# Kernel optimization log

Hardware: AMD Instinct MI355X
Metric: run time of the kernel (lower is better)

Reference implementation:

```python
import jax, jax.numpy as jnp
import numpy as np

NPOINT = 512
NSAMPLE = 32
RADIUS = 0.2


def furthest_point_sampling(pts, npoint):
    # pts: (B, N, 3) -> (B, npoint) int32 indices
    B, N, _ = pts.shape

    def step(carry, _):
        dist, far = carry  # (B,N), (B,)
        centroid = jnp.take_along_axis(pts, far[:, None, None], axis=1)  # (B,1,3)
        d2 = jnp.sum((pts - centroid) ** 2, axis=-1)  # (B,N)
        dist = jnp.minimum(dist, d2)
        nfar = jnp.argmax(dist, axis=-1).astype(jnp.int32)
        return (dist, nfar), far

    init = (jnp.full((B, N), 1e10, pts.dtype), jnp.zeros((B,), jnp.int32))
    _, idxs = jax.lax.scan(step, init, None, length=npoint)
    return idxs.T  # (B, npoint)


def ball_query(new_xyz, xyz, nsample, radius):
    # new_xyz: (B,S,3), xyz: (B,N,3) -> (B,S,nsample) int32
    N = xyz.shape[1]
    d2 = jnp.sum((new_xyz[:, :, None, :] - xyz[:, None, :, :]) ** 2, axis=-1)  # (B,S,N)
    ar = jnp.arange(N, dtype=jnp.int32)
    key = jnp.where(d2 < radius * radius, ar, N)  # valid idx, else sentinel N
    idx = jnp.sort(key, axis=-1)[..., :nsample]  # first nsample in-radius indices
    first = idx[..., :1]
    idx = jnp.where(idx == N, first, idx)  # pad with first valid (CUDA ball_query behavior)
    return jnp.minimum(idx, N - 1)


def group_points(feat, idx):
    # feat: (B,C,N), idx: (B,S,K) -> (B,C,S,K)
    return jax.vmap(lambda f, i: f[:, i])(feat, idx)


def pointnet_sa(xyz, features, W1, b1, W2, b2, W3, b3):
    xyz_t = jnp.transpose(xyz, (0, 2, 1))  # (B,N,3)
    fps_idx = furthest_point_sampling(xyz_t, NPOINT)  # (B,S)
    new_xyz = group_points(xyz, fps_idx[:, :, None])[..., 0]  # (B,3,S)
    idx = ball_query(jnp.transpose(new_xyz, (0, 2, 1)), xyz_t, NSAMPLE, RADIUS)  # (B,S,K)
    grouped_xyz = group_points(xyz, idx) - new_xyz[:, :, :, None]  # (B,3,S,K), centered
    grouped_feat = group_points(features, idx)  # (B,C,S,K)
    h = jnp.concatenate([grouped_xyz, grouped_feat], axis=1)  # (B,C+3,S,K)
    for W, b in ((W1, b1), (W2, b2), (W3, b3)):
        h = jax.nn.relu(jnp.einsum('oc,bcsk->bosk', W, h) + b[None, :, None, None])
    new_features = jnp.max(h, axis=3)  # (B,out,S)
    return new_xyz, new_features


def setup_inputs() -> dict:
    key = jax.random.key(0)
    ks = jax.random.split(key, 8)
    B, N, C = 16, 2048, 64
    return {
        'xyz': jax.random.uniform(ks[0], (B, 3, N), dtype=jnp.float32),
        'features': jax.random.normal(ks[1], (B, C, N), dtype=jnp.float32),
        'W1': jax.random.normal(ks[2], (64, 67), dtype=jnp.float32) * 0.1,
        'b1': jnp.zeros((64,), jnp.float32),
        'W2': jax.random.normal(ks[3], (128, 64), dtype=jnp.float32) * 0.1,
        'b2': jnp.zeros((128,), jnp.float32),
        'W3': jax.random.normal(ks[4], (256, 128), dtype=jnp.float32) * 0.1,
        'b3': jnp.zeros((256,), jnp.float32),
    }


def reference(xyz, features, W1, b1, W2, b2, W3, b3):
    return pointnet_sa(xyz, features, W1, b1, W2, b2, W3, b3)
```

## Files before the change

kernel.cpp:

```cpp
#include <hip/hip_runtime.h>

#define NB 16
#define NN 2048
#define NP 512
#define NS 32
#define NC 64

typedef _Float16 f16x8 __attribute__((ext_vector_type(8)));
typedef _Float16 f16x4 __attribute__((ext_vector_type(4)));
typedef float f32x4 __attribute__((ext_vector_type(4)));
typedef float f32x2 __attribute__((ext_vector_type(2)));

__device__ __forceinline__ float sqdist(float dx, float dy, float dz) {
  return __fadd_rn(__fadd_rn(__fmul_rn(dx, dx), __fmul_rn(dy, dy)), __fmul_rn(dz, dz));
}

__device__ __forceinline__ f32x2 pk_add(f32x2 a, f32x2 b) {
  f32x2 d;
  asm("v_pk_add_f32 %0, %1, %2" : "=v"(d) : "v"(a), "v"(b));
  return d;
}
__device__ __forceinline__ f32x2 pk_mul(f32x2 a, f32x2 b) {
  f32x2 d;
  asm("v_pk_mul_f32 %0, %1, %2" : "=v"(d) : "v"(a), "v"(b));
  return d;
}

template <int CTRL>
__device__ __forceinline__ float dppmaxf(float m) {
  int t = __builtin_amdgcn_update_dpp(0, __float_as_int(m), CTRL, 0xf, 0xf, true);
  return fmaxf(m, __int_as_float(t));
}

__global__ __launch_bounds__(256, 1) void front_kernel(
    const float* __restrict__ xyz, const float* __restrict__ feat,
    const float* __restrict__ W1, const float* __restrict__ W2, const float* __restrict__ W3,
    float* __restrict__ newxyz, _Float16* __restrict__ featF, float* __restrict__ xyzT,
    _Float16* __restrict__ W1f, _Float16* __restrict__ W2f, _Float16* __restrict__ W3f) {
  __shared__ __align__(16) char sm[32896];
  const int bid = blockIdx.x;
  const int t = threadIdx.x;

  if (bid >= 16) {
    if (bid == 528) {
      for (int i = t; i < 256 * 128; i += 256) {
        if (i < 64 * 96) {
          int o = i / 96, k = i - o * 96;
          float v = (k < 64) ? W1[o * 67 + 3 + k] : ((k < 67) ? W1[o * 67 + (k - 64)] : 0.f);
          W1f[i] = (_Float16)v;
        }
        if (i < 128 * 64) W2f[i] = (_Float16)W2[i];
        W3f[i] = (_Float16)W3[i];
      }
      return;
    }
    float(*tile)[65] = (float(*)[65])sm;
    const int pb = bid - 16;
    const int b = pb >> 5;
    const int n0 = (pb & 31) * 64;
    const int g = t >> 6, l = t & 63;
    if (g == 0) {
      int n = n0 + l;
      float4 q;
      q.x = xyz[(size_t)b * 3 * NN + n];
      q.y = xyz[(size_t)b * 3 * NN + NN + n];
      q.z = xyz[(size_t)b * 3 * NN + 2 * NN + n];
      q.w = 0.f;
      ((float4*)xyzT)[(size_t)b * NN + n] = q;
    }
#pragma unroll
    for (int r = 0; r < 16; ++r) {
      int c = g * 16 + r;
      tile[c][l] = feat[((size_t)b * NC + c) * NN + n0 + l];
    }
    __syncthreads();
#pragma unroll
    for (int r = 0; r < 16; ++r) {
      int nl = g * 16 + r;
      featF[((size_t)(b * NN + n0 + nl)) * NC + l] = (_Float16)tile[l][nl];
    }
    return;
  }

  const int b = bid;
  const int w = t >> 6;
  const float* X = xyz + (size_t)b * 3 * NN;
  float4* XL = (float4*)sm;
  uint2* ck = (uint2*)(sm + 32768);

  f32x2 px[4], py[4], pz[4], dist[4];
#pragma unroll
  for (int jj = 0; jj < 4; ++jj) {
    int n0 = t + 256 * jj, n1 = n0 + 1024;
    px[jj] = f32x2{X[n0], X[n1]};
    py[jj] = f32x2{X[NN + n0], X[NN + n1]};
    pz[jj] = f32x2{X[2 * NN + n0], X[2 * NN + n1]};
    dist[jj] = f32x2{1e10f, 1e10f};
    XL[n0] = make_float4(px[jj].x, py[jj].x, pz[jj].x, 0.f);
    XL[n1] = make_float4(px[jj].y, py[jj].y, pz[jj].y, 0.f);
  }
  float cx = X[0], cy = X[NN], cz = X[2 * NN];
  __syncthreads();
  int buf = 0;
  for (int i = 0; i < NP; ++i) {
    if (t == 0) {
      newxyz[b * 3 * NP + i] = cx;
      newxyz[b * 3 * NP + NP + i] = cy;
      newxyz[b * 3 * NP + 2 * NP + i] = cz;
    }
    const f32x2 ncx = f32x2{-cx, -cx}, ncy = f32x2{-cy, -cy}, ncz = f32x2{-cz, -cz};
    float hm[4];
#pragma unroll
    for (int jj = 0; jj < 4; ++jj) {
      f32x2 dx = pk_add(px[jj], ncx);
      f32x2 dy = pk_add(py[jj], ncy);
      f32x2 dz = pk_add(pz[jj], ncz);
      f32x2 s = pk_add(pk_add(pk_mul(dx, dx), pk_mul(dy, dy)), pk_mul(dz, dz));
      f32x2 d = dist[jj];
      d.x = fminf(d.x, s.x);
      d.y = fminf(d.y, s.y);
      dist[jj] = d;
      hm[jj] = fmaxf(d.x, d.y);
    }
    float m = fmaxf(fmaxf(hm[0], hm[1]), fmaxf(hm[2], hm[3]));
    m = dppmaxf<0x111>(m);
    m = dppmaxf<0x112>(m);
    m = dppmaxf<0x114>(m);
    m = dppmaxf<0x118>(m);
    m = dppmaxf<0x142>(m);
    m = dppmaxf<0x143>(m);
    const float vmax = __int_as_float(__builtin_amdgcn_readlane(__float_as_int(m), 63));
    unsigned long long mm[8];
#pragma unroll
    for (int jj = 0; jj < 4; ++jj) {
      mm[jj] = __ballot(dist[jj].x == vmax);
      mm[4 + jj] = __ballot(dist[jj].y == vmax);
    }
    unsigned nw = 0;
#pragma unroll
    for (int q = 7; q >= 0; --q)
      if (mm[q]) nw = 256u * (unsigned)q + (unsigned)(w << 6) + (unsigned)__builtin_ctzll(mm[q]);
    if ((t & 63) == 0) ck[buf * 4 + w] = make_uint2(__float_as_uint(vmax), nw);
    __syncthreads();
    uint4 c01 = *(const uint4*)&ck[buf * 4 + 0];
    uint4 c23 = *(const uint4*)&ck[buf * 4 + 2];
    unsigned v = c01.x, n = c01.y;
    if (c01.z > v || (c01.z == v && c01.w < n)) { v = c01.z; n = c01.w; }
    if (c23.x > v || (c23.x == v && c23.y < n)) { v = c23.x; n = c23.y; }
    if (c23.z > v || (c23.z == v && c23.w < n)) { v = c23.z; n = c23.w; }
    float4 c = XL[n];
    cx = c.x;
    cy = c.y;
    cz = c.z;
    buf ^= 1;
  }
}

#define HSTR 104
#define A1STR 72
#define A2STR 136
#define A1OFF 17408

__global__ __launch_bounds__(256) void mlp_kernel(
    const float* __restrict__ xyz, const float* __restrict__ xyzT,
    const _Float16* __restrict__ featF, const float* __restrict__ newxyz,
    const _Float16* __restrict__ W1f, const float* __restrict__ b1,
    const _Float16* __restrict__ W2f, const float* __restrict__ b2,
    const _Float16* __restrict__ W3f, const float* __restrict__ b3, float* __restrict__ out) {
  __shared__ _Float16 smem[17408 + 9216];
  __shared__ int idx_l[4][32];
  __shared__ float cxyz[4][4];
  _Float16* hT = smem;
  _Float16* a1T = smem + A1OFF;
  const int b = blockIdx.x;
  const int s0 = blockIdx.y * 4;
  const int t = threadIdx.x;
  const int lane = t & 63, w = t >> 6;

  {
    const float* X = xyz + (size_t)b * 3 * NN;
    const int sW = s0 + w;
    const float cxw = newxyz[b * 3 * NP + sW];
    const float cyw = newxyz[b * 3 * NP + NP + sW];
    const float czw = newxyz[b * 3 * NP + 2 * NP + sW];
    if (lane == 0) {
      cxyz[w][0] = cxw;
      cxyz[w][1] = cyw;
      cxyz[w][2] = czw;
    }
    const float r2 = (float)(0.2 * 0.2);
    int total = 0, first = 0;
    bool havefirst = false;
    for (int c0 = 0; c0 < NN; c0 += 64) {
      int n = c0 + lane;
      float d2 = sqdist(X[n] - cxw, X[NN + n] - cyw, X[2 * NN + n] - czw);
      bool hit = d2 < r2;
      unsigned long long mask = __ballot(hit);
      if (!havefirst && mask) {
        first = c0 + __builtin_ctzll(mask);
        havefirst = true;
      }
      if (hit) {
        int pos = total + (int)__popcll(mask & ((1ull << lane) - 1ull));
        if (pos < NS) idx_l[w][pos] = n;
      }
      total += (int)__popcll(mask);
      if (total >= NS) break;
    }
    if (total < NS && lane >= total && lane < NS) idx_l[w][lane] = first;
  }
  __syncthreads();

  {
    const int col = t & 127, hf = t >> 7;
    const int n = idx_l[col >> 5][col & 31];
    const _Float16* F = featF + (size_t)(b * NN + n) * NC;
#pragma unroll
    for (int j = 0; j < 4; ++j) {
      int p = hf * 4 + j;
      *(f16x8*)(&hT[col * HSTR + p * 8]) = *(const f16x8*)(F + p * 8);
    }
    if (hf == 0) {
      float4 pnt = ((const float4*)xyzT)[(size_t)b * NN + n];
      f16x8 v = {};
      v[0] = (_Float16)(pnt.x - cxyz[col >> 5][0]);
      v[1] = (_Float16)(pnt.y - cxyz[col >> 5][1]);
      v[2] = (_Float16)(pnt.z - cxyz[col >> 5][2]);
      *(f16x8*)(&hT[col * HSTR + 64]) = v;
    } else {
      f16x8 z = {};
      *(f16x8*)(&hT[col * HSTR + 72]) = z;
      *(f16x8*)(&hT[col * HSTR + 80]) = z;
      *(f16x8*)(&hT[col * HSTR + 88]) = z;
    }
  }
  __syncthreads();

  const int cl = lane & 15;
  const int kg = lane >> 4;

  {
    f32x4 acc[8];
    {
      f32x4 bb = *(const f32x4*)(b1 + w * 16 + kg * 4);
#pragma unroll
      for (int ct = 0; ct < 8; ++ct) acc[ct] = bb;
    }
#pragma unroll
    for (int ks = 0; ks < 3; ++ks) {
      f16x8 A = *(const f16x8*)(W1f + (w * 16 + cl) * 96 + ks * 32 + kg * 8);
#pragma unroll
      for (int ct = 0; ct < 8; ++ct) {
        f16x8 B = *(const f16x8*)(&hT[(ct * 16 + cl) * HSTR + ks * 32 + kg * 8]);
        acc[ct] = __builtin_amdgcn_mfma_f32_16x16x32_f16(A, B, acc[ct], 0, 0, 0);
      }
    }
#pragma unroll
    for (int ct = 0; ct < 8; ++ct) {
      f16x4 v;
#pragma unroll
      for (int i2 = 0; i2 < 4; ++i2) v[i2] = (_Float16)fmaxf(acc[ct][i2], 0.f);
      *(f16x4*)(&a1T[(ct * 16 + cl) * A1STR + w * 16 + kg * 4]) = v;
    }
  }
  __syncthreads();

  {
    f32x4 acc[2][8];
#pragma unroll
    for (int r = 0; r < 2; ++r) {
      f32x4 bb = *(const f32x4*)(b2 + w * 32 + r * 16 + kg * 4);
#pragma unroll
      for (int ct = 0; ct < 8; ++ct) acc[r][ct] = bb;
    }
#pragma unroll
    for (int ks = 0; ks < 2; ++ks) {
      f16x8 A0 = *(const f16x8*)(W2f + (w * 32 + cl) * 64 + ks * 32 + kg * 8);
      f16x8 A1 = *(const f16x8*)(W2f + (w * 32 + 16 + cl) * 64 + ks * 32 + kg * 8);
#pragma unroll
      for (int ct = 0; ct < 8; ++ct) {
        f16x8 B = *(const f16x8*)(&a1T[(ct * 16 + cl) * A1STR + ks * 32 + kg * 8]);
        acc[0][ct] = __builtin_amdgcn_mfma_f32_16x16x32_f16(A0, B, acc[0][ct], 0, 0, 0);
        acc[1][ct] = __builtin_amdgcn_mfma_f32_16x16x32_f16(A1, B, acc[1][ct], 0, 0, 0);
      }
    }
#pragma unroll
    for (int r = 0; r < 2; ++r)
#pragma unroll
      for (int ct = 0; ct < 8; ++ct) {
        f16x4 v;
#pragma unroll
        for (int i2 = 0; i2 < 4; ++i2) v[i2] = (_Float16)fmaxf(acc[r][ct][i2], 0.f);
        *(f16x4*)(&hT[(ct * 16 + cl) * A2STR + w * 32 + r * 16 + kg * 4]) = v;
      }
  }
  __syncthreads();

  float* out2 = out + NB * 3 * NP;
#pragma unroll
  for (int rh = 0; rh < 2; ++rh) {
    f32x4 acc[2][8];
#pragma unroll
    for (int r = 0; r < 2; ++r) {
      f32x4 bb = *(const f32x4*)(b3 + w * 64 + rh * 32 + r * 16 + kg * 4);
#pragma unroll
      for (int ct = 0; ct < 8; ++ct) acc[r][ct] = bb;
    }
#pragma unroll
    for (int ks = 0; ks < 4; ++ks) {
      f16x8 A0 = *(const f16x8*)(W3f + (w * 64 + rh * 32 + cl) * 128 + ks * 32 + kg * 8);
      f16x8 A1 = *(const f16x8*)(W3f + (w * 64 + rh * 32 + 16 + cl) * 128 + ks * 32 + kg * 8);
#pragma unroll
      for (int ct = 0; ct < 8; ++ct) {
        f16x8 B = *(const f16x8*)(&hT[(ct * 16 + cl) * A2STR + ks * 32 + kg * 8]);
        acc[0][ct] = __builtin_amdgcn_mfma_f32_16x16x32_f16(A0, B, acc[0][ct], 0, 0, 0);
        acc[1][ct] = __builtin_amdgcn_mfma_f32_16x16x32_f16(A1, B, acc[1][ct], 0, 0, 0);
      }
    }
#pragma unroll
    for (int r = 0; r < 2; ++r)
#pragma unroll
      for (int sl = 0; sl < 4; ++sl) {
        float vv[4];
#pragma unroll
        for (int i2 = 0; i2 < 4; ++i2) {
          float m0 = fmaxf(acc[r][sl * 2][i2], 0.f);
          float m1 = fmaxf(acc[r][sl * 2 + 1][i2], 0.f);
          float mv = fmaxf(m0, m1);
          mv = fmaxf(mv, __shfl_xor(mv, 1, 64));
          mv = fmaxf(mv, __shfl_xor(mv, 2, 64));
          mv = fmaxf(mv, __shfl_xor(mv, 4, 64));
          mv = fmaxf(mv, __shfl_xor(mv, 8, 64));
          vv[i2] = mv;
        }
        if (cl == 0) {
          int ob = w * 64 + rh * 32 + r * 16 + kg * 4;
#pragma unroll
          for (int i2 = 0; i2 < 4; ++i2)
            out2[((size_t)(b * 256 + ob + i2)) * NP + s0 + sl] = vv[i2];
        }
      }
  }
}

extern "C" void kernel_launch(void* const* d_in, const int* in_sizes, int n_in, void* d_out,
                              int out_size, void* d_ws, size_t ws_size, hipStream_t stream) {
  const float* xyz = (const float*)d_in[0];
  const float* feat = (const float*)d_in[1];
  const float* W1 = (const float*)d_in[2];
  const float* b1 = (const float*)d_in[3];
  const float* W2 = (const float*)d_in[4];
  const float* b2 = (const float*)d_in[5];
  const float* W3 = (const float*)d_in[6];
  const float* b3 = (const float*)d_in[7];
  float* out = (float*)d_out;
  char* ws = (char*)d_ws;
  float* xyzT = (float*)ws;
  _Float16* featF = (_Float16*)(ws + 524288);
  _Float16* W1f = (_Float16*)(ws + 4718592);
  _Float16* W2f = (_Float16*)(ws + 4730880);
  _Float16* W3f = (_Float16*)(ws + 4747264);

  hipLaunchKernelGGL(front_kernel, dim3(529), dim3(256), 0, stream, xyz, feat, W1, W2, W3, out,
                     featF, xyzT, W1f, W2f, W3f);
  hipLaunchKernelGGL(mlp_kernel, dim3(NB, 128), dim3(256), 0, stream, xyz, xyzT, featF, out, W1f,
                     b1, W2f, b2, W3f, b3, out);
}
```

Baseline: 388.6 us.

## Fuse FPS and MLP into persistent kernel with counter-based streaming of centroids

Merges the sampling/preprocessing kernel and the grouping+MLP kernel into one persistent kernel of 512 blocks. The 16 FPS blocks publish centroids every 64 iterations through release counters. The other blocks first do the feature transpose and weight conversion, then pull MLP work items from an atomic queue and spin-wait until the needed centroids exist. This lets ball query and the MLP run alongside the serial FPS loop instead of after it. The cost is spin-wait overhead, atomics, and reliance on all blocks being co-resident; it also adds a small init kernel to reset the counters.

```diff
diff --git a/kernel.cpp b/kernel.cpp
--- a/kernel.cpp
+++ b/kernel.cpp
@@ -5,6 +5,7 @@
 #define NP 512
 #define NS 32
 #define NC 64
+#define NWORK 496
 
 typedef _Float16 f16x8 __attribute__((ext_vector_type(8)));
 typedef _Float16 f16x4 __attribute__((ext_vector_type(4)));
@@ -32,17 +33,153 @@
   return fmaxf(m, __int_as_float(t));
 }
 
-__global__ __launch_bounds__(256, 1) void front_kernel(
+__device__ __forceinline__ unsigned ld_relax(const unsigned* p) {
+  return __hip_atomic_load(p, __ATOMIC_RELAXED, __HIP_MEMORY_SCOPE_AGENT);
+}
+__device__ __forceinline__ void waitge(const unsigned* p, unsigned need) {
+  if (ld_relax(p) < need) {
+    unsigned spins = 0;
+    while (ld_relax(p) < need) {
+      __builtin_amdgcn_s_sleep(8);
+      if (++spins > (1u << 22)) break;
+    }
+  }
+  (void)__hip_atomic_load(p, __ATOMIC_ACQUIRE, __HIP_MEMORY_SCOPE_AGENT);
+}
+
+__global__ void init_kernel(unsigned* ctr) {
+  if (threadIdx.x < 18) ctr[threadIdx.x * 16] = 0;
+}
+
+#define HSTR 104
+#define A1STR 72
+#define A2STR 136
+#define A1OFF 17408
+
+__global__ __launch_bounds__(256, 2) void fused_kernel(
     const float* __restrict__ xyz, const float* __restrict__ feat,
-    const float* __restrict__ W1, const float* __restrict__ W2, const float* __restrict__ W3,
-    float* __restrict__ newxyz, _Float16* __restrict__ featF, float* __restrict__ xyzT,
-    _Float16* __restrict__ W1f, _Float16* __restrict__ W2f, _Float16* __restrict__ W3f) {
-  __shared__ __align__(16) char sm[32896];
+    const float* __restrict__ W1, const float* __restrict__ b1, const float* __restrict__ W2,
+    const float* __restrict__ b2, const float* __restrict__ W3, const float* __restrict__ b3,
+    float* __restrict__ out, _Float16* __restrict__ featF, float* __restrict__ xyzT,
+    _Float16* __restrict__ W1f, _Float16* __restrict__ W2f, _Float16* __restrict__ W3f,
+    unsigned* __restrict__ ctr) {
+  __shared__ __align__(16) char sm[53824];
+  __shared__ unsigned mitem;
   const int bid = blockIdx.x;
   const int t = threadIdx.x;
-
-  if (bid >= 16) {
-    if (bid == 528) {
+  float* newxyz = out;
+
+  if (bid < NB) {
+    const int b = bid;
+    const int w = t >> 6;
+    const float* X = xyz + (size_t)b * 3 * NN;
+    float4* XL = (float4*)sm;
+    uint2* ck = (uint2*)(sm + 32768);
+
+    f32x2 px[4], py[4], pz[4], dist[4];
+#pragma unroll
+    for (int jj = 0; jj < 4; ++jj) {
+      int n0 = t + 256 * jj, n1 = n0 + 1024;
+      px[jj] = f32x2{X[n0], X[n1]};
+      py[jj] = f32x2{X[NN + n0], X[NN + n1]};
+      pz[jj] = f32x2{X[2 * NN + n0], X[2 * NN + n1]};
+      dist[jj] = f32x2{1e10f, 1e10f};
+      XL[n0] = make_float4(px[jj].x, py[jj].x, pz[jj].x, 0.f);
+      XL[n1] = make_float4(px[jj].y, py[jj].y, pz[jj].y, 0.f);
+    }
+    float cx = X[0], cy = X[NN], cz = X[2 * NN];
+    __syncthreads();
+    int buf = 0;
+    for (int i = 0; i < NP; ++i) {
+      if (t == 0) {
+        __hip_atomic_store(&newxyz[b * 3 * NP + i], cx, __ATOMIC_RELAXED,
+                           __HIP_MEMORY_SCOPE_AGENT);
+        __hip_atomic_store(&newxyz[b * 3 * NP + NP + i], cy, __ATOMIC_RELAXED,
+                           __HIP_MEMORY_SCOPE_AGENT);
+        __hip_atomic_store(&newxyz[b * 3 * NP + 2 * NP + i], cz, __ATOMIC_RELAXED,
+                           __HIP_MEMORY_SCOPE_AGENT);
+        if ((i & 63) == 63)
+          __hip_atomic_store(&ctr[b * 16], (unsigned)(i + 1), __ATOMIC_RELEASE,
+                             __HIP_MEMORY_SCOPE_AGENT);
+      }
+      const f32x2 ncx = f32x2{-cx, -cx}, ncy = f32x2{-cy, -cy}, ncz = f32x2{-cz, -cz};
+      float hm[4];
+#pragma unroll
+      for (int jj = 0; jj < 4; ++jj) {
+        f32x2 dx = pk_add(px[jj], ncx);
+        f32x2 dy = pk_add(py[jj], ncy);
+        f32x2 dz = pk_add(pz[jj], ncz);
+        f32x2 s = pk_add(pk_add(pk_mul(dx, dx), pk_mul(dy, dy)), pk_mul(dz, dz));
+        f32x2 d = dist[jj];
+        d.x = fminf(d.x, s.x);
+        d.y = fminf(d.y, s.y);
+        dist[jj] = d;
+        hm[jj] = fmaxf(d.x, d.y);
+      }
+      float m = fmaxf(fmaxf(hm[0], hm[1]), fmaxf(hm[2], hm[3]));
+      m = dppmaxf<0x111>(m);
+      m = dppmaxf<0x112>(m);
+      m = dppmaxf<0x114>(m);
+      m = dppmaxf<0x118>(m);
+      m = dppmaxf<0x142>(m);
+      m = dppmaxf<0x143>(m);
+      const float vmax = __int_as_float(__builtin_amdgcn_readlane(__float_as_int(m), 63));
+      unsigned long long mm[8];
+#pragma unroll
+      for (int jj = 0; jj < 4; ++jj) {
+        mm[jj] = __ballot(dist[jj].x == vmax);
+        mm[4 + jj] = __ballot(dist[jj].y == vmax);
+      }
+      unsigned nw = 0;
+#pragma unroll
+      for (int q = 7; q >= 0; --q)
+        if (mm[q]) nw = 256u * (unsigned)q + (unsigned)(w << 6) + (unsigned)__builtin_ctzll(mm[q]);
+      if ((t & 63) == 0) ck[buf * 4 + w] = make_uint2(__float_as_uint(vmax), nw);
+      __syncthreads();
+      uint4 c01 = *(const uint4*)&ck[buf * 4 + 0];
+      uint4 c23 = *(const uint4*)&ck[buf * 4 + 2];
+      unsigned v = c01.x, n = c01.y;
+      if (c01.z > v || (c01.z == v && c01.w < n)) { v = c01.z; n = c01.w; }
+      if (c23.x > v || (c23.x == v && c23.y < n)) { v = c23.x; n = c23.y; }
+      if (c23.z > v || (c23.z == v && c23.w < n)) { v = c23.z; n = c23.w; }
+      float4 c = XL[n];
+      cx = c.x;
+      cy = c.y;
+      cz = c.z;
+      buf ^= 1;
+    }
+  } else {
+    const int wid = bid - NB;
+    for (int rep = 0; rep < 2; ++rep) {
+      int p = wid + rep * NWORK;
+      if (p >= 512) break;
+      float(*tile)[65] = (float(*)[65])sm;
+      const int b = p >> 5;
+      const int n0 = (p & 31) * 64;
+      const int g = t >> 6, l = t & 63;
+      if (g == 0) {
+        int n = n0 + l;
+        float4 q;
+        q.x = xyz[(size_t)b * 3 * NN + n];
+        q.y = xyz[(size_t)b * 3 * NN + NN + n];
+        q.z = xyz[(size_t)b * 3 * NN + 2 * NN + n];
+        q.w = 0.f;
+        ((float4*)xyzT)[(size_t)b * NN + n] = q;
+      }
+      __syncthreads();
+#pragma unroll
+      for (int r = 0; r < 16; ++r) {
+        int c = g * 16 + r;
+        tile[c][l] = feat[((size_t)b * NC + c) * NN + n0 + l];
+      }
+      __syncthreads();
+#pragma unroll
+      for (int r = 0; r < 16; ++r) {
+        int nl = g * 16 + r;
+        featF[((size_t)(b * NN + n0 + nl)) * NC + l] = (_Float16)tile[l][nl];
+      }
+    }
+    if (wid == 31) {
       for (int i = t; i < 256 * 128; i += 256) {
         if (i < 64 * 96) {
           int o = i / 96, k = i - o * 96;
@@ -52,294 +189,199 @@
         if (i < 128 * 64) W2f[i] = (_Float16)W2[i];
         W3f[i] = (_Float16)W3[i];
       }
-      return;
-    }
-    float(*tile)[65] = (float(*)[65])sm;
-    const int pb = bid - 16;
-    const int b = pb >> 5;
-    const int n0 = (pb & 31) * 64;
-    const int g = t >> 6, l = t & 63;
-    if (g == 0) {
-      int n = n0 + l;
-      float4 q;
-      q.x = xyz[(size_t)b * 3 * NN + n];
-      q.y = xyz[(size_t)b * 3 * NN + NN + n];
-      q.z = xyz[(size_t)b * 3 * NN + 2 * NN + n];
-      q.w = 0.f;
-      ((float4*)xyzT)[(size_t)b * NN + n] = q;
-    }
-#pragma unroll
-    for (int r = 0; r < 16; ++r) {
-      int c = g * 16 + r;
-      tile[c][l] = feat[((size_t)b * NC + c) * NN + n0 + l];
-    }
-    __syncthreads();
-#pragma unroll
-    for (int r = 0; r < 16; ++r) {
-      int nl = g * 16 + r;
-      featF[((size_t)(b * NN + n0 + nl)) * NC + l] = (_Float16)tile[l][nl];
-    }
-    return;
+    }
+    __syncthreads();
+    if (t == 0)
+      (void)__hip_atomic_fetch_add(&ctr[16 * 16], 1u, __ATOMIC_RELEASE,
+                                   __HIP_MEMORY_SCOPE_AGENT);
   }
 
-  const int b = bid;
-  const int w = t >> 6;
-  const float* X = xyz + (size_t)b * 3 * NN;
-  float4* XL = (float4*)sm;
-  uint2* ck = (uint2*)(sm + 32768);
-
-  f32x2 px[4], py[4], pz[4], dist[4];
-#pragma unroll
-  for (int jj = 0; jj < 4; ++jj) {
-    int n0 = t + 256 * jj, n1 = n0 + 1024;
-    px[jj] = f32x2{X[n0], X[n1]};
-    py[jj] = f32x2{X[NN + n0], X[NN + n1]};
-    pz[jj] = f32x2{X[2 * NN + n0], X[2 * NN + n1]};
-    dist[jj] = f32x2{1e10f, 1e10f};
-    XL[n0] = make_float4(px[jj].x, py[jj].x, pz[jj].x, 0.f);
-    XL[n1] = make_float4(px[jj].y, py[jj].y, pz[jj].y, 0.f);
-  }
-  float cx = X[0], cy = X[NN], cz = X[2 * NN];
+  if (t == 0) waitge(&ctr[16 * 16], NWORK);
   __syncthreads();
-  int buf = 0;
-  for (int i = 0; i < NP; ++i) {
-    if (t == 0) {
-      newxyz[b * 3 * NP + i] = cx;
-      newxyz[b * 3 * NP + NP + i] = cy;
-      newxyz[b * 3 * NP + 2 * NP + i] = cz;
-    }
-    const f32x2 ncx = f32x2{-cx, -cx}, ncy = f32x2{-cy, -cy}, ncz = f32x2{-cz, -cz};
-    float hm[4];
-#pragma unroll
-    for (int jj = 0; jj < 4; ++jj) {
-      f32x2 dx = pk_add(px[jj], ncx);
-      f32x2 dy = pk_add(py[jj], ncy);
-      f32x2 dz = pk_add(pz[jj], ncz);
-      f32x2 s = pk_add(pk_add(pk_mul(dx, dx), pk_mul(dy, dy)), pk_mul(dz, dz));
-      f32x2 d = dist[jj];
-      d.x = fminf(d.x, s.x);
-      d.y = fminf(d.y, s.y);
-      dist[jj] = d;
-      hm[jj] = fmaxf(d.x, d.y);
-    }
-    float m = fmaxf(fmaxf(hm[0], hm[1]), fmaxf(hm[2], hm[3]));
-    m = dppmaxf<0x111>(m);
-    m = dppmaxf<0x112>(m);
-    m = dppmaxf<0x114>(m);
-    m = dppmaxf<0x118>(m);
-    m = dppmaxf<0x142>(m);
-    m = dppmaxf<0x143>(m);
-    const float vmax = __int_as_float(__builtin_amdgcn_readlane(__float_as_int(m), 63));
-    unsigned long long mm[8];
-#pragma unroll
-    for (int jj = 0; jj < 4; ++jj) {
-      mm[jj] = __ballot(dist[jj].x == vmax);
-      mm[4 + jj] = __ballot(dist[jj].y == vmax);
-    }
-    unsigned nw = 0;
-#pragma unroll
-    for (int q = 7; q >= 0; --q)
-      if (mm[q]) nw = 256u * (unsigned)q + (unsigned)(w << 6) + (unsigned)__builtin_ctzll(mm[q]);
-    if ((t & 63) == 0) ck[buf * 4 + w] = make_uint2(__float_as_uint(vmax), nw);
-    __syncthreads();
-    uint4 c01 = *(const uint4*)&ck[buf * 4 + 0];
-    uint4 c23 = *(const uint4*)&ck[buf * 4 + 2];
-    unsigned v = c01.x, n = c01.y;
-    if (c01.z > v || (c01.z == v && c01.w < n)) { v = c01.z; n = c01.w; }
-    if (c23.x > v || (c23.x == v && c23.y < n)) { v = c23.x; n = c23.y; }
-    if (c23.z > v || (c23.z == v && c23.w < n)) { v = c23.z; n = c23.w; }
-    float4 c = XL[n];
-    cx = c.x;
-    cy = c.y;
-    cz = c.z;
-    buf ^= 1;
-  }
-}
-
-#define HSTR 104
-#define A1STR 72
-#define A2STR 136
-#define A1OFF 17408
-
-__global__ __launch_bounds__(256) void mlp_kernel(
-    const float* __restrict__ xyz, const float* __restrict__ xyzT,
-    const _Float16* __restrict__ featF, const float* __restrict__ newxyz,
-    const _Float16* __restrict__ W1f, const float* __restrict__ b1,
-    const _Float16* __restrict__ W2f, const float* __restrict__ b2,
-    const _Float16* __restrict__ W3f, const float* __restrict__ b3, float* __restrict__ out) {
-  __shared__ _Float16 smem[17408 + 9216];
-  __shared__ int idx_l[4][32];
-  __shared__ float cxyz[4][4];
-  _Float16* hT = smem;
-  _Float16* a1T = smem + A1OFF;
-  const int b = blockIdx.x;
-  const int s0 = blockIdx.y * 4;
-  const int t = threadIdx.x;
+
+  _Float16* hT = (_Float16*)sm;
+  _Float16* a1T = (_Float16*)(sm) + A1OFF;
+  int(*idx_l)[32] = (int(*)[32])(sm + 53248);
+  float(*cxyz)[4] = (float(*)[4])(sm + 53760);
   const int lane = t & 63, w = t >> 6;
-
-  {
-    const float* X = xyz + (size_t)b * 3 * NN;
-    const int sW = s0 + w;
-    const float cxw = newxyz[b * 3 * NP + sW];
-    const float cyw = newxyz[b * 3 * NP + NP + sW];
-    const float czw = newxyz[b * 3 * NP + 2 * NP + sW];
-    if (lane == 0) {
-      cxyz[w][0] = cxw;
-      cxyz[w][1] = cyw;
-      cxyz[w][2] = czw;
-    }
-    const float r2 = (float)(0.2 * 0.2);
-    int total = 0, first = 0;
-    bool havefirst = false;
-    for (int c0 = 0; c0 < NN; c0 += 64) {
-      int n = c0 + lane;
-      float d2 = sqdist(X[n] - cxw, X[NN + n] - cyw, X[2 * NN + n] - czw);
-      bool hit = d2 < r2;
-      unsigned long long mask = __ballot(hit);
-      if (!havefirst && mask) {
-        first = c0 + __builtin_ctzll(mask);
-        havefirst = true;
-      }
-      if (hit) {
-        int pos = total + (int)__popcll(mask & ((1ull << lane) - 1ull));
-        if (pos < NS) idx_l[w][pos] = n;
-      }
-      total += (int)__popcll(mask);
-      if (total >= NS) break;
-    }
-    if (total < NS && lane >= total && lane < NS) idx_l[w][lane] = first;
-  }
-  __syncthreads();
-
-  {
-    const int col = t & 127, hf = t >> 7;
-    const int n = idx_l[col >> 5][col & 31];
-    const _Float16* F = featF + (size_t)(b * NN + n) * NC;
-#pragma unroll
-    for (int j = 0; j < 4; ++j) {
-      int p = hf * 4 + j;
-      *(f16x8*)(&hT[col * HSTR + p * 8]) = *(const f16x8*)(F + p * 8);
-    }
-    if (hf == 0) {
-      float4 pnt = ((const float4*)xyzT)[(size_t)b * NN + n];
-      f16x8 v = {};
-      v[0] = (_Float16)(pnt.x - cxyz[col >> 5][0]);
-      v[1] = (_Float16)(pnt.y - cxyz[col >> 5][1]);
-      v[2] = (_Float16)(pnt.z - cxyz[col >> 5][2]);
-      *(f16x8*)(&hT[col * HSTR + 64]) = v;
-    } else {
-      f16x8 z = {};
-      *(f16x8*)(&hT[col * HSTR + 72]) = z;
-      *(f16x8*)(&hT[col * HSTR + 80]) = z;
-      *(f16x8*)(&hT[col * HSTR + 88]) = z;
-    }
-  }
-  __syncthreads();
-
   const int cl = lane & 15;
   const int kg = lane >> 4;
-
-  {
-    f32x4 acc[8];
+  float* out2 = out + NB * 3 * NP;
+
+  for (;;) {
+    if (t == 0)
+      mitem = __hip_atomic_fetch_add(&ctr[17 * 16], 1u, __ATOMIC_RELAXED,
+                                     __HIP_MEMORY_SCOPE_AGENT);
+    __syncthreads();
+    const unsigned m = mitem;
+    if (m >= (unsigned)(NB * 128)) break;
+    const int b = (int)(m & 15u);
+    const int sg = (int)(m >> 4);
+    const int s0 = sg * 4;
+    if (t == 0) waitge(&ctr[b * 16], (unsigned)(s0 + 4));
+    __syncthreads();
+
     {
-      f32x4 bb = *(const f32x4*)(b1 + w * 16 + kg * 4);
-#pragma unroll
-      for (int ct = 0; ct < 8; ++ct) acc[ct] = bb;
-    }
-#pragma unroll
-    for (int ks = 0; ks < 3; ++ks) {
-      f16x8 A = *(const f16x8*)(W1f + (w * 16 + cl) * 96 + ks * 32 + kg * 8);
-#pragma unroll
-      for (int ct = 0; ct < 8; ++ct) {
-        f16x8 B = *(const f16x8*)(&hT[(ct * 16 + cl) * HSTR + ks * 32 + kg * 8]);
-        acc[ct] = __builtin_amdgcn_mfma_f32_16x16x32_f16(A, B, acc[ct], 0, 0, 0);
-      }
-    }
-#pragma unroll
-    for (int ct = 0; ct < 8; ++ct) {
-      f16x4 v;
-#pragma unroll
-      for (int i2 = 0; i2 < 4; ++i2) v[i2] = (_Float16)fmaxf(acc[ct][i2], 0.f);
-      *(f16x4*)(&a1T[(ct * 16 + cl) * A1STR + w * 16 + kg * 4]) = v;
-    }
-  }
-  __syncthreads();
-
-  {
-    f32x4 acc[2][8];
-#pragma unroll
-    for (int r = 0; r < 2; ++r) {
-      f32x4 bb = *(const f32x4*)(b2 + w * 32 + r * 16 + kg * 4);
-#pragma unroll
-      for (int ct = 0; ct < 8; ++ct) acc[r][ct] = bb;
-    }
-#pragma unroll
-    for (int ks = 0; ks < 2; ++ks) {
-      f16x8 A0 = *(const f16x8*)(W2f + (w * 32 + cl) * 64 + ks * 32 + kg * 8);
-      f16x8 A1 = *(const f16x8*)(W2f + (w * 32 + 16 + cl) * 64 + ks * 32 + kg * 8);
-#pragma unroll
-      for (int ct = 0; ct < 8; ++ct) {
-        f16x8 B = *(const f16x8*)(&a1T[(ct * 16 + cl) * A1STR + ks * 32 + kg * 8]);
-        acc[0][ct] = __builtin_amdgcn_mfma_f32_16x16x32_f16(A0, B, acc[0][ct], 0, 0, 0);
-        acc[1][ct] = __builtin_amdgcn_mfma_f32_16x16x32_f16(A1, B, acc[1][ct], 0, 0, 0);
-      }
-    }
-#pragma unroll
-    for (int r = 0; r < 2; ++r)
+      const float* X = xyz + (size_t)b * 3 * NN;
+      const int sW = s0 + w;
+      const float cxw = newxyz[b * 3 * NP + sW];
+      const float cyw = newxyz[b * 3 * NP + NP + sW];
+      const float czw = newxyz[b * 3 * NP + 2 * NP + sW];
+      if (lane == 0) {
+        cxyz[w][0] = cxw;
+        cxyz[w][1] = cyw;
+        cxyz[w][2] = czw;
+      }
+      const float r2 = (float)(0.2 * 0.2);
+      int total = 0, first = 0;
+      bool havefirst = false;
+      for (int c0 = 0; c0 < NN; c0 += 64) {
+        int n = c0 + lane;
+        float d2 = sqdist(X[n] - cxw, X[NN + n] - cyw, X[2 * NN + n] - czw);
+        bool hit = d2 < r2;
+        unsigned long long mask = __ballot(hit);
+        if (!havefirst && mask) {
+          first = c0 + __builtin_ctzll(mask);
+          havefirst = true;
+        }
+        if (hit) {
+          int pos = total + (int)__popcll(mask & ((1ull << lane) - 1ull));
+          if (pos < NS) idx_l[w][pos] = n;
+        }
+        total += (int)__popcll(mask);
+        if (total >= NS) break;
+      }
+      if (total < NS && lane >= total && lane < NS) idx_l[w][lane] = first;
+    }
+    __syncthreads();
+
+    {
+      const int col = t & 127, hf = t >> 7;
+      const int n = idx_l[col >> 5][col & 31];
+      const _Float16* F = featF + (size_t)(b * NN + n) * NC;
+#pragma unroll
+      for (int j = 0; j < 4; ++j) {
+        int p = hf * 4 + j;
+        *(f16x8*)(&hT[col * HSTR + p * 8]) = *(const f16x8*)(F + p * 8);
+      }
+      if (hf == 0) {
+        float4 pnt = ((const float4*)xyzT)[(size_t)b * NN + n];
+        f16x8 v = {};
+        v[0] = (_Float16)(pnt.x - cxyz[col >> 5][0]);
+        v[1] = (_Float16)(pnt.y - cxyz[col >> 5][1]);
+        v[2] = (_Float16)(pnt.z - cxyz[col >> 5][2]);
+        *(f16x8*)(&hT[col * HSTR + 64]) = v;
+      } else {
+        f16x8 z = {};
+        *(f16x8*)(&hT[col * HSTR + 72]) = z;
+        *(f16x8*)(&hT[col * HSTR + 80]) = z;
+        *(f16x8*)(&hT[col * HSTR + 88]) = z;
+      }
+    }
+    __syncthreads();
+
+    {
+      f32x4 acc[8];
+      {
+        f32x4 bb = *(const f32x4*)(b1 + w * 16 + kg * 4);
+#pragma unroll
+        for (int ct = 0; ct < 8; ++ct) acc[ct] = bb;
+      }
+#pragma unroll
+      for (int ks = 0; ks < 3; ++ks) {
+        f16x8 A = *(const f16x8*)(W1f + (w * 16 + cl) * 96 + ks * 32 + kg * 8);
+#pragma unroll
+        for (int ct = 0; ct < 8; ++ct) {
+          f16x8 B = *(const f16x8*)(&hT[(ct * 16 + cl) * HSTR + ks * 32 + kg * 8]);
+          acc[ct] = __builtin_amdgcn_mfma_f32_16x16x32_f16(A, B, acc[ct], 0, 0, 0);
+        }
+      }
 #pragma unroll
       for (int ct = 0; ct < 8; ++ct) {
         f16x4 v;
 #pragma unroll
-        for (int i2 = 0; i2 < 4; ++i2) v[i2] = (_Float16)fmaxf(acc[r][ct][i2], 0.f);
-        *(f16x4*)(&hT[(ct * 16 + cl) * A2STR + w * 32 + r * 16 + kg * 4]) = v;
-      }
-  }
-  __syncthreads();
-
-  float* out2 = out + NB * 3 * NP;
-#pragma unroll
-  for (int rh = 0; rh < 2; ++rh) {
-    f32x4 acc[2][8];
-#pragma unroll
-    for (int r = 0; r < 2; ++r) {
-      f32x4 bb = *(const f32x4*)(b3 + w * 64 + rh * 32 + r * 16 + kg * 4);
-#pragma unroll
-      for (int ct = 0; ct < 8; ++ct) acc[r][ct] = bb;
-    }
-#pragma unroll
-    for (int ks = 0; ks < 4; ++ks) {
-      f16x8 A0 = *(const f16x8*)(W3f + (w * 64 + rh * 32 + cl) * 128 + ks * 32 + kg * 8);
-      f16x8 A1 = *(const f16x8*)(W3f + (w * 64 + rh * 32 + 16 + cl) * 128 + ks * 32 + kg * 8);
-#pragma unroll
-      for (int ct = 0; ct < 8; ++ct) {
-        f16x8 B = *(const f16x8*)(&hT[(ct * 16 + cl) * A2STR + ks * 32 + kg * 8]);
-        acc[0][ct] = __builtin_amdgcn_mfma_f32_16x16x32_f16(A0, B, acc[0][ct], 0, 0, 0);
-        acc[1][ct] = __builtin_amdgcn_mfma_f32_16x16x32_f16(A1, B, acc[1][ct], 0, 0, 0);
-      }
-    }
-#pragma unroll
-    for (int r = 0; r < 2; ++r)
-#pragma unroll
-      for (int sl = 0; sl < 4; ++sl) {
-        float vv[4];
-#pragma unroll
-        for (int i2 = 0; i2 < 4; ++i2) {
-          float m0 = fmaxf(acc[r][sl * 2][i2], 0.f);
-          float m1 = fmaxf(acc[r][sl * 2 + 1][i2], 0.f);
-          float mv = fmaxf(m0, m1);
-          mv = fmaxf(mv, __shfl_xor(mv, 1, 64));
-          mv = fmaxf(mv, __shfl_xor(mv, 2, 64));
-          mv = fmaxf(mv, __shfl_xor(mv, 4, 64));
-          mv = fmaxf(mv, __shfl_xor(mv, 8, 64));
-          vv[i2] = mv;
-        }
-        if (cl == 0) {
-          int ob = w * 64 + rh * 32 + r * 16 + kg * 4;
-#pragma unroll
-          for (int i2 = 0; i2 < 4; ++i2)
-            out2[((size_t)(b * 256 + ob + i2)) * NP + s0 + sl] = vv[i2];
-        }
-      }
+        for (int i2 = 0; i2 < 4; ++i2) v[i2] = (_Float16)fmaxf(acc[ct][i2], 0.f);
+        *(f16x4*)(&a1T[(ct * 16 + cl) * A1STR + w * 16 + kg * 4]) = v;
+      }
+    }
+    __syncthreads();
+
+    {
+      f32x4 acc[2][8];
+#pragma unroll
+      for (int r = 0; r < 2; ++r) {
+        f32x4 bb = *(const f32x4*)(b2 + w * 32 + r * 16 + kg * 4);
+#pragma unroll
+        for (int ct = 0; ct < 8; ++ct) acc[r][ct] = bb;
+      }
+#pragma unroll
+      for (int ks = 0; ks < 2; ++ks) {
+        f16x8 A0 = *(const f16x8*)(W2f + (w * 32 + cl) * 64 + ks * 32 + kg * 8);
+        f16x8 A1 = *(const f16x8*)(W2f + (w * 32 + 16 + cl) * 64 + ks * 32 + kg * 8);
+#pragma unroll
+        for (int ct = 0; ct < 8; ++ct) {
+          f16x8 B = *(const f16x8*)(&a1T[(ct * 16 + cl) * A1STR + ks * 32 + kg * 8]);
+          acc[0][ct] = __builtin_amdgcn_mfma_f32_16x16x32_f16(A0, B, acc[0][ct], 0, 0, 0);
+          acc[1][ct] = __builtin_amdgcn_mfma_f32_16x16x32_f16(A1, B, acc[1][ct], 0, 0, 0);
+        }
+      }
+#pragma unroll
+      for (int r = 0; r < 2; ++r)
+#pragma unroll
+        for (int ct = 0; ct < 8; ++ct) {
+          f16x4 v;
+#pragma unroll
+          for (int i2 = 0; i2 < 4; ++i2) v[i2] = (_Float16)fmaxf(acc[r][ct][i2], 0.f);
+          *(f16x4*)(&hT[(ct * 16 + cl) * A2STR + w * 32 + r * 16 + kg * 4]) = v;
+        }
+    }
+    __syncthreads();
+
+#pragma unroll
+    for (int rh = 0; rh < 2; ++rh) {
+      f32x4 acc[2][8];
+#pragma unroll
+      for (int r = 0; r < 2; ++r) {
+        f32x4 bb = *(const f32x4*)(b3 + w * 64 + rh * 32 + r * 16 + kg * 4);
+#pragma unroll
+        for (int ct = 0; ct < 8; ++ct) acc[r][ct] = bb;
+      }
+#pragma unroll
+      for (int ks = 0; ks < 4; ++ks) {
+        f16x8 A0 = *(const f16x8*)(W3f + (w * 64 + rh * 32 + cl) * 128 + ks * 32 + kg * 8);
+        f16x8 A1 = *(const f16x8*)(W3f + (w * 64 + rh * 32 + 16 + cl) * 128 + ks * 32 + kg * 8);
+#pragma unroll
+        for (int ct = 0; ct < 8; ++ct) {
+          f16x8 B = *(const f16x8*)(&hT[(ct * 16 + cl) * A2STR + ks * 32 + kg * 8]);
+          acc[0][ct] = __builtin_amdgcn_mfma_f32_16x16x32_f16(A0, B, acc[0][ct], 0, 0, 0);
+          acc[1][ct] = __builtin_amdgcn_mfma_f32_16x16x32_f16(A1, B, acc[1][ct], 0, 0, 0);
+        }
+      }
+#pragma unroll
+      for (int r = 0; r < 2; ++r)
+#pragma unroll
+        for (int sl = 0; sl < 4; ++sl) {
+          float vv[4];
+#pragma unroll
+          for (int i2 = 0; i2 < 4; ++i2) {
+            float m0 = fmaxf(acc[r][sl * 2][i2], 0.f);
+            float m1 = fmaxf(acc[r][sl * 2 + 1][i2], 0.f);
+            float mv = fmaxf(m0, m1);
+            mv = fmaxf(mv, __shfl_xor(mv, 1, 64));
+            mv = fmaxf(mv, __shfl_xor(mv, 2, 64));
+            mv = fmaxf(mv, __shfl_xor(mv, 4, 64));
+            mv = fmaxf(mv, __shfl_xor(mv, 8, 64));
+            vv[i2] = mv;
+          }
+          if (cl == 0) {
+            int ob = w * 64 + rh * 32 + r * 16 + kg * 4;
+#pragma unroll
+            for (int i2 = 0; i2 < 4; ++i2)
+              out2[((size_t)(b * 256 + ob + i2)) * NP + s0 + sl] = vv[i2];
+          }
+        }
+    }
+    __syncthreads();
   }
 }
 
@@ -360,9 +402,9 @@
   _Float16* W1f = (_Float16*)(ws + 4718592);
   _Float16* W2f = (_Float16*)(ws + 4730880);
   _Float16* W3f = (_Float16*)(ws + 4747264);
-
-  hipLaunchKernelGGL(front_kernel, dim3(529), dim3(256), 0, stream, xyz, feat, W1, W2, W3, out,
-                     featF, xyzT, W1f, W2f, W3f);
-  hipLaunchKernelGGL(mlp_kernel, dim3(NB, 128), dim3(256), 0, stream, xyz, xyzT, featF, out, W1f,
-                     b1, W2f, b2, W3f, b3, out);
-}
+  unsigned* ctr = (unsigned*)(ws + 4812800);
+
+  hipLaunchKernelGGL(init_kernel, dim3(1), dim3(64), 0, stream, ctr);
+  hipLaunchKernelGGL(fused_kernel, dim3(512), dim3(256), 0, stream, xyz, feat, W1, b1, W2, b2, W3,
+                     b3, out, featF, xyzT, W1f, W2f, W3f, ctr);
+}
```

Result: faster. 333.8 us (median of 2 runs) (-14.1%).
